# Performance work log

Measured on AMD Instinct MI355X. Metric: run time of the kernel, lower is better.

Reference implementation:

```python
import jax, jax.numpy as jnp
import numpy as np

HIDDEN = 32
IN_DIM = 4
WARMUP = 29  # steps using ground-truth input; afterwards feed back own output


def _gru_cell(x, h, w_ih, w_hh, b_ih, b_hh):
    # PyTorch GRUCell math. x: [B, 4], h: [B, 32]
    gi = x @ w_ih.T + b_ih          # [B, 96]
    gh = h @ w_hh.T + b_hh          # [B, 96]
    i_r, i_z, i_n = jnp.split(gi, 3, axis=-1)
    h_r, h_z, h_n = jnp.split(gh, 3, axis=-1)
    r = jax.nn.sigmoid(i_r + h_r)
    z = jax.nn.sigmoid(i_z + h_z)
    n = jnp.tanh(i_n + r * h_n)
    return (1.0 - z) * n + z * h


def setup_inputs() -> dict:
    key = jax.random.key(0)
    ks = jax.random.split(key, 8)
    B, T = 131072, 60
    s_ih = 1.0 / np.sqrt(HIDDEN)
    return {
        "input": jax.random.normal(ks[0], (B, IN_DIM, T), dtype=jnp.float32),
        "w_ih": jax.random.uniform(ks[1], (3 * HIDDEN, IN_DIM), jnp.float32, -s_ih, s_ih),
        "w_hh": jax.random.uniform(ks[2], (3 * HIDDEN, HIDDEN), jnp.float32, -s_ih, s_ih),
        "b_ih": jax.random.uniform(ks[3], (3 * HIDDEN,), jnp.float32, -s_ih, s_ih),
        "b_hh": jax.random.uniform(ks[4], (3 * HIDDEN,), jnp.float32, -s_ih, s_ih),
        "w_lin": jax.random.uniform(ks[5], (IN_DIM, HIDDEN), jnp.float32, -s_ih, s_ih),
        "b_lin": jax.random.uniform(ks[6], (IN_DIM,), jnp.float32, -s_ih, s_ih),
    }


def reference(input, w_ih, w_hh, b_ih, b_hh, w_lin, b_lin):
    B, _, T = input.shape
    xs = jnp.transpose(input, (2, 0, 1))  # [T, B, 4]
    h0 = jnp.zeros((B, HIDDEN), dtype=input.dtype)
    out0 = jnp.zeros((B, IN_DIM), dtype=input.dtype)

    def step(carry, xi):
        h, prev_out, h28 = carry
        x_t, i = xi
        inp = jnp.where(i < WARMUP, x_t, prev_out)
        h = _gru_cell(inp, h, w_ih, w_hh, b_ih, b_hh)
        out = h @ w_lin.T + b_lin
        h28 = jnp.where(i == WARMUP - 1, h, h28)
        return (h, out, h28), out

    (_, _, h28), outs = jax.lax.scan(step, (h0, out0, h0), (xs, jnp.arange(T)))
    outputs = jnp.transpose(outs, (1, 2, 0))  # [B, 4, T] to match torch.stack(dim=2)
    return outputs, [h28]
```

## Files before the change

kernel.cpp:

```cpp
#include <hip/hip_runtime.h>

#define T_STEPS 60
#define WARMUP  29
#define HID     32
#define CT      240

__device__ __forceinline__ float fexp2(float x) { return __builtin_amdgcn_exp2f(x); }
__device__ __forceinline__ float frcp(float x)  { return __builtin_amdgcn_rcpf(x); }
__device__ __forceinline__ float sigmoid_f(float x) {
    return frcp(1.0f + fexp2(-1.4426950408889634f * x));
}
__device__ __forceinline__ float tanh_f(float x) {
    float e = fexp2(2.8853900817779268f * x);
    return 1.0f - 2.0f * frcp(e + 1.0f);
}

#define PIN(x) asm("" : "+v"(x))

template<int K>
__device__ __forceinline__ float bcast(float x) {
    return __int_as_float(__builtin_amdgcn_ds_swizzle(__float_as_int(x), (K << 5)));
}

#define GATHER32(v, x) do { \
    v[0]  = bcast<0>(x);  v[1]  = bcast<1>(x);  v[2]  = bcast<2>(x);  v[3]  = bcast<3>(x);  \
    v[4]  = bcast<4>(x);  v[5]  = bcast<5>(x);  v[6]  = bcast<6>(x);  v[7]  = bcast<7>(x);  \
    v[8]  = bcast<8>(x);  v[9]  = bcast<9>(x);  v[10] = bcast<10>(x); v[11] = bcast<11>(x); \
    v[12] = bcast<12>(x); v[13] = bcast<13>(x); v[14] = bcast<14>(x); v[15] = bcast<15>(x); \
    v[16] = bcast<16>(x); v[17] = bcast<17>(x); v[18] = bcast<18>(x); v[19] = bcast<19>(x); \
    v[20] = bcast<20>(x); v[21] = bcast<21>(x); v[22] = bcast<22>(x); v[23] = bcast<23>(x); \
    v[24] = bcast<24>(x); v[25] = bcast<25>(x); v[26] = bcast<26>(x); v[27] = bcast<27>(x); \
    v[28] = bcast<28>(x); v[29] = bcast<29>(x); v[30] = bcast<30>(x); v[31] = bcast<31>(x); \
} while (0)

#define GRU_STEP() do {                                                        \
    float gr = bgr, gz = bgz, gni = bgni, gnh = bgnh;                          \
    _Pragma("unroll")                                                          \
    for (int c = 0; c < 4; ++c) {                                              \
        gr  = __builtin_fmaf(wir[c], u[c], gr);                                \
        gz  = __builtin_fmaf(wiz[c], u[c], gz);                                \
        gni = __builtin_fmaf(win[c], u[c], gni);                               \
    }                                                                          \
    _Pragma("unroll")                                                          \
    for (int k = 0; k < HID; ++k) {                                            \
        gr  = __builtin_fmaf(whr[k], v[k], gr);                                \
        gz  = __builtin_fmaf(whz[k], v[k], gz);                                \
        gnh = __builtin_fmaf(whn[k], v[k], gnh);                               \
    }                                                                          \
    float r = sigmoid_f(gr);                                                   \
    float z = sigmoid_f(gz);                                                   \
    float n = tanh_f(__builtin_fmaf(r, gnh, gni));                             \
    x = __builtin_fmaf(z, x - n, n);                                           \
    GATHER32(v, x);                                                            \
    o = bl;                                                                    \
    _Pragma("unroll")                                                          \
    for (int k = 0; k < HID; ++k) o = __builtin_fmaf(wlr[k], v[k], o);         \
} while (0)

__global__ __launch_bounds__(256, 2) void gru_fused(
    const float* __restrict__ in,
    const float* w_ih,  const float* w_hh,
    const float* b_ih,  const float* b_hh,
    const float* w_lin, const float* b_lin,
    float* out, float* h28out, int B)
{
    const int lane = threadIdx.x & 63;
    const int j    = lane & 31;
    const int wv   = threadIdx.x >> 6;
    const int s    = lane >> 5;
    const int b    = blockIdx.x * 8 + wv * 2 + s;

    float whr[HID], whz[HID], whn[HID], wlr[HID];
    float wir[4], wiz[4], win[4];
    {
        const float4* pr = (const float4*)(w_hh + (size_t)j * HID);
        const float4* pz = (const float4*)(w_hh + (size_t)(HID + j) * HID);
        const float4* pn = (const float4*)(w_hh + (size_t)(2 * HID + j) * HID);
        const float4* pl = (const float4*)(w_lin + (size_t)(j & 3) * HID);
#pragma unroll
        for (int q = 0; q < 8; ++q) {
            float4 a = pr[q];
            whr[4*q] = a.x; whr[4*q+1] = a.y; whr[4*q+2] = a.z; whr[4*q+3] = a.w;
            float4 c = pz[q];
            whz[4*q] = c.x; whz[4*q+1] = c.y; whz[4*q+2] = c.z; whz[4*q+3] = c.w;
            float4 d = pn[q];
            whn[4*q] = d.x; whn[4*q+1] = d.y; whn[4*q+2] = d.z; whn[4*q+3] = d.w;
            float4 e = pl[q];
            wlr[4*q] = e.x; wlr[4*q+1] = e.y; wlr[4*q+2] = e.z; wlr[4*q+3] = e.w;
        }
        float4 a = ((const float4*)w_ih)[j];
        wir[0] = a.x; wir[1] = a.y; wir[2] = a.z; wir[3] = a.w;
        float4 c = ((const float4*)w_ih)[HID + j];
        wiz[0] = c.x; wiz[1] = c.y; wiz[2] = c.z; wiz[3] = c.w;
        float4 d = ((const float4*)w_ih)[2 * HID + j];
        win[0] = d.x; win[1] = d.y; win[2] = d.z; win[3] = d.w;
    }
    float bgr  = b_ih[j]           + b_hh[j];
    float bgz  = b_ih[HID + j]     + b_hh[HID + j];
    float bgni = b_ih[2 * HID + j];
    float bgnh = b_hh[2 * HID + j];
    float bl   = b_lin[j & 3];

#pragma unroll
    for (int k = 0; k < HID; ++k) { PIN(whr[k]); PIN(whz[k]); PIN(whn[k]); PIN(wlr[k]); }
#pragma unroll
    for (int c = 0; c < 4; ++c) { PIN(wir[c]); PIN(wiz[c]); PIN(win[c]); }
    PIN(bgr); PIN(bgz); PIN(bgni); PIN(bgnh); PIN(bl);

    float v[HID], u[4];
    float x = 0.0f, o = 0.0f;
#pragma unroll
    for (int k = 0; k < HID; ++k) v[k] = 0.0f;

    const float* pin  = in  + (size_t)b * CT;
    float*       pout = out + (size_t)b * CT + (j & 3) * T_STEPS;

#pragma unroll 1
    for (int t = 0; t < WARMUP; ++t) {
        u[0] = pin[t];
        u[1] = pin[60 + t];
        u[2] = pin[120 + t];
        u[3] = pin[180 + t];
        GRU_STEP();
        if (j < 4) pout[t] = o;
    }

    h28out[(size_t)b * HID + j] = x;

#pragma unroll 1
    for (int t = WARMUP; t < T_STEPS; ++t) {
        u[0] = bcast<0>(o);
        u[1] = bcast<1>(o);
        u[2] = bcast<2>(o);
        u[3] = bcast<3>(o);
        GRU_STEP();
        if (j < 4) pout[t] = o;
    }
}

extern "C" void kernel_launch(void* const* d_in, const int* in_sizes, int n_in,
                              void* d_out, int out_size, void* d_ws, size_t ws_size,
                              hipStream_t stream) {
    const float* input = (const float*)d_in[0];
    float* w_ih  = (float*)d_in[1];
    float* w_hh  = (float*)d_in[2];
    float* b_ih  = (float*)d_in[3];
    float* b_hh  = (float*)d_in[4];
    float* w_lin = (float*)d_in[5];
    float* b_lin = (float*)d_in[6];

    const int B = in_sizes[0] / CT;
    float* out = (float*)d_out;
    float* h28 = out + (size_t)B * CT;
    (void)d_ws; (void)ws_size;

    hipLaunchKernelGGL(gru_fused, dim3(B / 8), dim3(256), 0, stream,
                       input, w_ih, w_hh, b_ih, b_hh, w_lin, b_lin, out, h28, B);
}
```

Measured before the change: 1.617 ms.

## Split GRU gate work across both wave halves, one batch row per wavefront

Each wavefront now handles one batch row instead of two. The lower 32 lanes compute the r and z gates, and the upper 32 lanes compute the n-gate hidden part and the output projection. Partial results are exchanged with ds_bpermute, which halves the per-lane weight registers and allows three blocks per SM instead of two. The next step's input is also prefetched one step ahead. The cost is twice as many wavefronts and extra cross-lane permutes on the serial dependency chain of each step.

```diff
diff --git a/kernel.cpp b/kernel.cpp
--- a/kernel.cpp
+++ b/kernel.cpp
@@ -16,48 +16,57 @@
 }
 
 #define PIN(x) asm("" : "+v"(x))
+#define PIN_ALL() do {                                                         \
+    _Pragma("unroll") for (int k_ = 0; k_ < HID; ++k_) { PIN(wa[k_]); PIN(wb[k_]); } \
+    _Pragma("unroll") for (int c_ = 0; c_ < 4; ++c_) { PIN(wi1[c_]); PIN(wi2[c_]); PIN(wi3[c_]); } \
+    PIN(b1); PIN(b2); PIN(b3); PIN(b4);                                        \
+} while (0)
 
 template<int K>
-__device__ __forceinline__ float bcast(float x) {
+__device__ __forceinline__ float swz(float x) {
     return __int_as_float(__builtin_amdgcn_ds_swizzle(__float_as_int(x), (K << 5)));
+}
+__device__ __forceinline__ float bperm(int idx, float x) {
+    return __int_as_float(__builtin_amdgcn_ds_bpermute(idx, __float_as_int(x)));
 }
 
 #define GATHER32(v, x) do { \
-    v[0]  = bcast<0>(x);  v[1]  = bcast<1>(x);  v[2]  = bcast<2>(x);  v[3]  = bcast<3>(x);  \
-    v[4]  = bcast<4>(x);  v[5]  = bcast<5>(x);  v[6]  = bcast<6>(x);  v[7]  = bcast<7>(x);  \
-    v[8]  = bcast<8>(x);  v[9]  = bcast<9>(x);  v[10] = bcast<10>(x); v[11] = bcast<11>(x); \
-    v[12] = bcast<12>(x); v[13] = bcast<13>(x); v[14] = bcast<14>(x); v[15] = bcast<15>(x); \
-    v[16] = bcast<16>(x); v[17] = bcast<17>(x); v[18] = bcast<18>(x); v[19] = bcast<19>(x); \
-    v[20] = bcast<20>(x); v[21] = bcast<21>(x); v[22] = bcast<22>(x); v[23] = bcast<23>(x); \
-    v[24] = bcast<24>(x); v[25] = bcast<25>(x); v[26] = bcast<26>(x); v[27] = bcast<27>(x); \
-    v[28] = bcast<28>(x); v[29] = bcast<29>(x); v[30] = bcast<30>(x); v[31] = bcast<31>(x); \
+    v[0]  = swz<0>(x);  v[1]  = swz<1>(x);  v[2]  = swz<2>(x);  v[3]  = swz<3>(x);  \
+    v[4]  = swz<4>(x);  v[5]  = swz<5>(x);  v[6]  = swz<6>(x);  v[7]  = swz<7>(x);  \
+    v[8]  = swz<8>(x);  v[9]  = swz<9>(x);  v[10] = swz<10>(x); v[11] = swz<11>(x); \
+    v[12] = swz<12>(x); v[13] = swz<13>(x); v[14] = swz<14>(x); v[15] = swz<15>(x); \
+    v[16] = swz<16>(x); v[17] = swz<17>(x); v[18] = swz<18>(x); v[19] = swz<19>(x); \
+    v[20] = swz<20>(x); v[21] = swz<21>(x); v[22] = swz<22>(x); v[23] = swz<23>(x); \
+    v[24] = swz<24>(x); v[25] = swz<25>(x); v[26] = swz<26>(x); v[27] = swz<27>(x); \
+    v[28] = swz<28>(x); v[29] = swz<29>(x); v[30] = swz<30>(x); v[31] = swz<31>(x); \
 } while (0)
 
-#define GRU_STEP() do {                                                        \
-    float gr = bgr, gz = bgz, gni = bgni, gnh = bgnh;                          \
-    _Pragma("unroll")                                                          \
-    for (int c = 0; c < 4; ++c) {                                              \
-        gr  = __builtin_fmaf(wir[c], u[c], gr);                                \
-        gz  = __builtin_fmaf(wiz[c], u[c], gz);                                \
-        gni = __builtin_fmaf(win[c], u[c], gni);                               \
-    }                                                                          \
+#define BODY() do {                                                            \
+    PIN_ALL();                                                                 \
+    float a1 = b1, a2 = b2, a3 = b3;                                           \
+    a1 = __builtin_fmaf(wi1[0], u0, a1); a2 = __builtin_fmaf(wi2[0], u0, a2); a3 = __builtin_fmaf(wi3[0], u0, a3); \
+    a1 = __builtin_fmaf(wi1[1], u1, a1); a2 = __builtin_fmaf(wi2[1], u1, a2); a3 = __builtin_fmaf(wi3[1], u1, a3); \
+    a1 = __builtin_fmaf(wi1[2], u2, a1); a2 = __builtin_fmaf(wi2[2], u2, a2); a3 = __builtin_fmaf(wi3[2], u2, a3); \
+    a1 = __builtin_fmaf(wi1[3], u3, a1); a2 = __builtin_fmaf(wi2[3], u3, a2); a3 = __builtin_fmaf(wi3[3], u3, a3); \
     _Pragma("unroll")                                                          \
     for (int k = 0; k < HID; ++k) {                                            \
-        gr  = __builtin_fmaf(whr[k], v[k], gr);                                \
-        gz  = __builtin_fmaf(whz[k], v[k], gz);                                \
-        gnh = __builtin_fmaf(whn[k], v[k], gnh);                               \
+        a1 = __builtin_fmaf(wa[k], v[k], a1);                                  \
+        a2 = __builtin_fmaf(wb[k], v[k], a2);                                  \
     }                                                                          \
-    float r = sigmoid_f(gr);                                                   \
-    float z = sigmoid_f(gz);                                                   \
-    float n = tanh_f(__builtin_fmaf(r, gnh, gni));                             \
-    x = __builtin_fmaf(z, x - n, n);                                           \
-    GATHER32(v, x);                                                            \
-    o = bl;                                                                    \
+    float gnhx = bperm(idxHi, a1);     \
+    float gnix = bperm(idxHi, a3);     \
+    float r = sigmoid_f(a1);                                                   \
+    float z = sigmoid_f(a2);                                                   \
+    float n = tanh_f(__builtin_fmaf(r, gnhx, gnix));                           \
+    x = __builtin_fmaf(z, x - n, n);               \
+    float xx = bperm(idxLo, x);               \
+    GATHER32(v, xx);                          \
+    og = b4;                                                                   \
     _Pragma("unroll")                                                          \
-    for (int k = 0; k < HID; ++k) o = __builtin_fmaf(wlr[k], v[k], o);         \
+    for (int k = 0; k < HID; ++k) og = __builtin_fmaf(wb[k], v[k], og);        \
 } while (0)
 
-__global__ __launch_bounds__(256, 2) void gru_fused(
+__global__ __launch_bounds__(256, 3) void gru_fused(
     const float* __restrict__ in,
     const float* w_ih,  const float* w_hh,
     const float* b_ih,  const float* b_hh,
@@ -66,75 +75,70 @@
 {
     const int lane = threadIdx.x & 63;
     const int j    = lane & 31;
+    const int hb   = lane >> 5;
     const int wv   = threadIdx.x >> 6;
-    const int s    = lane >> 5;
-    const int b    = blockIdx.x * 8 + wv * 2 + s;
+    const int b    = blockIdx.x * 4 + wv;
 
-    float whr[HID], whz[HID], whn[HID], wlr[HID];
-    float wir[4], wiz[4], win[4];
+    float wa[HID], wb[HID], wi1[4], wi2[4], wi3[4];
     {
-        const float4* pr = (const float4*)(w_hh + (size_t)j * HID);
-        const float4* pz = (const float4*)(w_hh + (size_t)(HID + j) * HID);
-        const float4* pn = (const float4*)(w_hh + (size_t)(2 * HID + j) * HID);
-        const float4* pl = (const float4*)(w_lin + (size_t)(j & 3) * HID);
+        const float4* pa = (const float4*)(w_hh + (size_t)(hb ? (2 * HID + j) : j) * HID);
+        const float4* pb = hb ? (const float4*)(w_lin + (size_t)(j & 3) * HID)
+                              : (const float4*)(w_hh + (size_t)(HID + j) * HID);
 #pragma unroll
         for (int q = 0; q < 8; ++q) {
-            float4 a = pr[q];
-            whr[4*q] = a.x; whr[4*q+1] = a.y; whr[4*q+2] = a.z; whr[4*q+3] = a.w;
-            float4 c = pz[q];
-            whz[4*q] = c.x; whz[4*q+1] = c.y; whz[4*q+2] = c.z; whz[4*q+3] = c.w;
-            float4 d = pn[q];
-            whn[4*q] = d.x; whn[4*q+1] = d.y; whn[4*q+2] = d.z; whn[4*q+3] = d.w;
-            float4 e = pl[q];
-            wlr[4*q] = e.x; wlr[4*q+1] = e.y; wlr[4*q+2] = e.z; wlr[4*q+3] = e.w;
+            float4 A = pa[q];
+            wa[4*q] = A.x; wa[4*q+1] = A.y; wa[4*q+2] = A.z; wa[4*q+3] = A.w;
+            float4 Bv = pb[q];
+            wb[4*q] = Bv.x; wb[4*q+1] = Bv.y; wb[4*q+2] = Bv.z; wb[4*q+3] = Bv.w;
         }
-        float4 a = ((const float4*)w_ih)[j];
-        wir[0] = a.x; wir[1] = a.y; wir[2] = a.z; wir[3] = a.w;
-        float4 c = ((const float4*)w_ih)[HID + j];
-        wiz[0] = c.x; wiz[1] = c.y; wiz[2] = c.z; wiz[3] = c.w;
-        float4 d = ((const float4*)w_ih)[2 * HID + j];
-        win[0] = d.x; win[1] = d.y; win[2] = d.z; win[3] = d.w;
+        float4 r1 = ((const float4*)w_ih)[j];
+        float4 r2 = ((const float4*)w_ih)[HID + j];
+        float4 r3 = ((const float4*)w_ih)[2 * HID + j];
+        wi1[0] = hb ? 0.0f : r1.x; wi1[1] = hb ? 0.0f : r1.y;
+        wi1[2] = hb ? 0.0f : r1.z; wi1[3] = hb ? 0.0f : r1.w;
+        wi2[0] = hb ? 0.0f : r2.x; wi2[1] = hb ? 0.0f : r2.y;
+        wi2[2] = hb ? 0.0f : r2.z; wi2[3] = hb ? 0.0f : r2.w;
+        wi3[0] = hb ? r3.x : 0.0f; wi3[1] = hb ? r3.y : 0.0f;
+        wi3[2] = hb ? r3.z : 0.0f; wi3[3] = hb ? r3.w : 0.0f;
     }
-    float bgr  = b_ih[j]           + b_hh[j];
-    float bgz  = b_ih[HID + j]     + b_hh[HID + j];
-    float bgni = b_ih[2 * HID + j];
-    float bgnh = b_hh[2 * HID + j];
-    float bl   = b_lin[j & 3];
+    float b1 = hb ? b_hh[2 * HID + j] : (b_ih[j] + b_hh[j]);
+    float b2 = hb ? 0.0f              : (b_ih[HID + j] + b_hh[HID + j]);
+    float b3 = hb ? b_ih[2 * HID + j] : 0.0f;
+    float b4 = hb ? b_lin[j & 3]      : 0.0f;
 
-#pragma unroll
-    for (int k = 0; k < HID; ++k) { PIN(whr[k]); PIN(whz[k]); PIN(whn[k]); PIN(wlr[k]); }
-#pragma unroll
-    for (int c = 0; c < 4; ++c) { PIN(wir[c]); PIN(wiz[c]); PIN(win[c]); }
-    PIN(bgr); PIN(bgz); PIN(bgni); PIN(bgnh); PIN(bl);
+    const int idxLo = j << 2;
+    const int idxHi = (j + 32) << 2;
+    const bool doO   = (hb == 1) && (j < 4);
+    const bool doH28 = (hb == 0);
 
-    float v[HID], u[4];
-    float x = 0.0f, o = 0.0f;
+    float v[HID];
+    float u0, u1, u2, u3, x = 0.0f, og = 0.0f;
 #pragma unroll
     for (int k = 0; k < HID; ++k) v[k] = 0.0f;
 
     const float* pin  = in  + (size_t)b * CT;
-    float*       pout = out + (size_t)b * CT + (j & 3) * T_STEPS;
+    float*       pout = out + (size_t)b * CT + j * T_STEPS;
 
+    u0 = pin[0]; u1 = pin[60]; u2 = pin[120]; u3 = pin[180];
 #pragma unroll 1
     for (int t = 0; t < WARMUP; ++t) {
-        u[0] = pin[t];
-        u[1] = pin[60 + t];
-        u[2] = pin[120 + t];
-        u[3] = pin[180 + t];
-        GRU_STEP();
-        if (j < 4) pout[t] = o;
+        float n0 = 0.0f, n1 = 0.0f, n2 = 0.0f, n3 = 0.0f;
+        if (t + 1 < WARMUP) {
+            n0 = pin[t + 1]; n1 = pin[61 + t]; n2 = pin[121 + t]; n3 = pin[181 + t];
+        }
+        BODY();
+        if (doO) pout[t] = og;
+        u0 = n0; u1 = n1; u2 = n2; u3 = n3;
     }
 
-    h28out[(size_t)b * HID + j] = x;
+    if (doH28) h28out[(size_t)b * HID + j] = x;
 
 #pragma unroll 1
     for (int t = WARMUP; t < T_STEPS; ++t) {
-        u[0] = bcast<0>(o);
-        u[1] = bcast<1>(o);
-        u[2] = bcast<2>(o);
-        u[3] = bcast<3>(o);
-        GRU_STEP();
-        if (j < 4) pout[t] = o;
+        float oo = bperm(idxHi, og);
+        u0 = swz<0>(oo); u1 = swz<1>(oo); u2 = swz<2>(oo); u3 = swz<3>(oo);
+        BODY();
+        if (doO) pout[t] = og;
     }
 }
 
@@ -154,6 +158,6 @@
     float* h28 = out + (size_t)B * CT;
     (void)d_ws; (void)ws_size;
 
-    hipLaunchKernelGGL(gru_fused, dim3(B / 8), dim3(256), 0, stream,
+    hipLaunchKernelGGL(gru_fused, dim3(B / 4), dim3(256), 0, stream,
                        input, w_ih, w_hh, b_ih, b_hh, w_lin, b_lin, out, h28, B);
 }
```

Result: slower. 2.255 ms (+39.4%).
